# Performance work log

Measured on AMD Instinct MI355X. Metric: run time of the kernel, lower is better.

## Reference

```python
import jax, jax.numpy as jnp
import numpy as np

B, S, D, H = 4, 1024, 1024, 16
HD = D // H  # head_dim = 64


def setup_inputs() -> dict:
    key = jax.random.key(0)
    ks = jax.random.split(key, 12)
    inp = {
        "query": jax.random.normal(ks[0], (B, S, D), jnp.float32),
        "key": jax.random.normal(ks[1], (B, S, D), jnp.float32),
        "value": jax.random.normal(ks[2], (B, S, D), jnp.float32),
        # padding mask: 0 = masked, 1 = keep; broadcastable to [B,H,Sq,Sk]
        "mask": jax.random.randint(ks[3], (B, 1, 1, S), 0, 2, jnp.int32),
        # Dense params (Glorot-ish scale)
        "Wq": jax.random.normal(ks[4], (D, D), jnp.float32) / np.sqrt(D),
        "bq": jnp.zeros((D,), jnp.float32),
        "Wk": jax.random.normal(ks[5], (D, D), jnp.float32) / np.sqrt(D),
        "bk": jnp.zeros((D,), jnp.float32),
        "Wv": jax.random.normal(ks[6], (D, D), jnp.float32) / np.sqrt(D),
        "bv": jnp.zeros((D,), jnp.float32),
        "Wo": jax.random.normal(ks[7], (D, D), jnp.float32) / np.sqrt(D),
        "bo": jnp.zeros((D,), jnp.float32),
    }
    return inp


def _split_heads(x):
    # [B, S, D] -> [B, H, S, HD]
    b, s, _ = x.shape
    return x.reshape(b, s, H, HD).transpose(0, 2, 1, 3)


def reference(query, key, value, mask, Wq, bq, Wk, bk, Wv, bv, Wo, bo):
    q = _split_heads(query @ Wq + bq)   # [B,H,S,HD]
    k = _split_heads(key @ Wk + bk)
    v = _split_heads(value @ Wv + bv)

    scale = jnp.sqrt(jnp.asarray(HD, q.dtype))
    energy = jnp.einsum("bhqd,bhkd->bhqk", q, k) / scale  # [B,H,S,S]
    energy = jnp.where(mask == 0, jnp.asarray(-1e10, energy.dtype), energy)
    attention = jax.nn.softmax(energy, axis=-1)
    # dropout is identity at inference
    x = jnp.einsum("bhqk,bhkd->bhqd", attention, v)       # [B,H,S,HD]
    x = x.transpose(0, 2, 1, 3).reshape(query.shape[0], -1, H * HD)  # [B,S,D]
    outputs = x @ Wo + bo
    return outputs, attention
```

## Files before the change

kernel.cpp:

```cpp
#include <hip/hip_runtime.h>

typedef short short8  __attribute__((ext_vector_type(8)));
typedef short short4v __attribute__((ext_vector_type(4)));
typedef float float4v __attribute__((ext_vector_type(4)));
typedef int   int4v   __attribute__((ext_vector_type(4)));

__device__ __forceinline__ short f2bf(float f) {
    unsigned u = __builtin_bit_cast(unsigned, f);
    u += 0x7fff + ((u >> 16) & 1);
    return (short)(u >> 16);
}

__device__ __forceinline__ void gl_lds16(const void* g, void* l) {
    __builtin_amdgcn_global_load_lds(
        (const __attribute__((address_space(1))) void*)g,
        (__attribute__((address_space(3))) void*)l, 16, 0, 0);
}

__global__ __launch_bounds__(256) void prep(
    const float* __restrict__ W0, const float* __restrict__ W1,
    const float* __restrict__ W2, const float* __restrict__ W3,
    short* __restrict__ T0, short* __restrict__ T1,
    short* __restrict__ T2, short* __restrict__ T3,
    const float* __restrict__ qf, const float* __restrict__ kf,
    const float* __restrict__ vf,
    short* __restrict__ Qb, short* __restrict__ Kb, short* __restrict__ Vb)
{
    __shared__ short Tl[64 * 72];
    const int tid = threadIdx.x;
    if (blockIdx.x >= 1024) {
        int cid = blockIdx.x - 1024;
        int arr = cid >> 11;
        const float* src = arr == 0 ? qf : arr == 1 ? kf : vf;
        short*       dst = arr == 0 ? Qb : arr == 1 ? Kb : Vb;
        size_t base = ((size_t)(cid & 2047) * 256 + tid) * 8;
        float4v v0 = *(const float4v*)&src[base];
        float4v v1 = *(const float4v*)&src[base + 4];
        short8 o = {f2bf(v0[0]), f2bf(v0[1]), f2bf(v0[2]), f2bf(v0[3]),
                    f2bf(v1[0]), f2bf(v1[1]), f2bf(v1[2]), f2bf(v1[3])};
        *(short8*)&dst[base] = o;
        return;
    }
    const int mat = blockIdx.x >> 8;
    const int t   = blockIdx.x & 255;
    const int k0 = (t >> 4) * 64, n0 = (t & 15) * 64;
    const float* W = mat == 0 ? W0 : mat == 1 ? W1 : mat == 2 ? W2 : W3;
    short*       T = mat == 0 ? T0 : mat == 1 ? T1 : mat == 2 ? T2 : T3;
    #pragma unroll
    for (int i = 0; i < 4; i++) {
        int c = tid + i * 256;
        int row = c >> 4, c4 = (c & 15) * 4;
        float4v v = *(const float4v*)&W[(size_t)(k0 + row) * 1024 + n0 + c4];
        short4v s = {f2bf(v[0]), f2bf(v[1]), f2bf(v[2]), f2bf(v[3])};
        *(short4v*)&Tl[row * 72 + c4] = s;
    }
    __syncthreads();
    #pragma unroll
    for (int i = 0; i < 2; i++) {
        int c = tid + i * 256;
        int nrow = c >> 3, k8 = (c & 7) * 8;
        short8 v;
        #pragma unroll
        for (int e = 0; e < 8; e++) v[e] = Tl[(k8 + e) * 72 + nrow];
        *(short8*)&T[(size_t)(n0 + nrow) * 1024 + k0 + k8] = v;
    }
}

template<int CMODE>
__global__ __launch_bounds__(256) void gemm128(
    const short* __restrict__ A, const short* __restrict__ Bt,
    const float* __restrict__ bias, void* __restrict__ Cv,
    int M, int N, int K)
{
    __shared__ short As[128 * 64];
    __shared__ short Bs[64 * 64];
    const int tid = threadIdx.x;
    const int w = tid >> 6, lid = tid & 63, quad = lid >> 4, l15 = lid & 15;
    const int wr = w >> 1, wc = w & 1;
    const int m0 = blockIdx.x * 128, n0 = blockIdx.y * 64;
    const int lrow = lid >> 3;
    const int lcb  = lid & 7;

    float4v acc[4][2];
    #pragma unroll
    for (int i = 0; i < 4; i++)
        #pragma unroll
        for (int j = 0; j < 2; j++) acc[i][j] = (float4v){0.f, 0.f, 0.f, 0.f};

    for (int kb = 0; kb < K; kb += 64) {
        #pragma unroll
        for (int p = 0; p < 4; p++) {
            int chunk = p * 4 + w;
            int row = chunk * 8 + lrow;
            int cb = lcb ^ (row & 7);
            gl_lds16(&A[(size_t)(m0 + row) * K + kb + cb * 8], &As[chunk * 512]);
        }
        #pragma unroll
        for (int p = 0; p < 2; p++) {
            int chunk = p * 4 + w;
            int row = chunk * 8 + lrow;
            int cb = lcb ^ (row & 7);
            gl_lds16(&Bt[(size_t)(n0 + row) * K + kb + cb * 8], &Bs[chunk * 512]);
        }
        __syncthreads();

        short8 af[4][2], bfr[2][2];
        #pragma unroll
        for (int i = 0; i < 4; i++) {
            int row = wr * 64 + i * 16 + l15;
            int sw = row & 7;
            #pragma unroll
            for (int h = 0; h < 2; h++)
                af[i][h] = *(short8*)&As[row * 64 + ((h * 4 + quad) ^ sw) * 8];
        }
        #pragma unroll
        for (int j = 0; j < 2; j++) {
            int row = wc * 32 + j * 16 + l15;
            int sw = row & 7;
            #pragma unroll
            for (int h = 0; h < 2; h++)
                bfr[j][h] = *(short8*)&Bs[row * 64 + ((h * 4 + quad) ^ sw) * 8];
        }
        #pragma unroll
        for (int i = 0; i < 4; i++)
            #pragma unroll
            for (int j = 0; j < 2; j++) {
                acc[i][j] = __builtin_amdgcn_mfma_f32_16x16x32_bf16(
                    af[i][0], bfr[j][0], acc[i][j], 0, 0, 0);
                acc[i][j] = __builtin_amdgcn_mfma_f32_16x16x32_bf16(
                    af[i][1], bfr[j][1], acc[i][j], 0, 0, 0);
            }
        __syncthreads();
    }

    #pragma unroll
    for (int j = 0; j < 2; j++) {
        int n = n0 + wc * 32 + j * 16 + l15;
        float bj = bias[n];
        #pragma unroll
        for (int i = 0; i < 4; i++) {
            if constexpr (CMODE == 2) {
                short* Vt = (short*)Cv;
                int b = m0 >> 10;
                int sbase = (m0 & 1023) + wr * 64 + i * 16 + quad * 4;
                short4v sv;
                #pragma unroll
                for (int r = 0; r < 4; r++) sv[r] = f2bf(acc[i][j][r] + bj);
                *(short4v*)&Vt[(size_t)b * 1048576 + (size_t)n * 1024 + sbase] = sv;
            } else {
                #pragma unroll
                for (int r = 0; r < 4; r++) {
                    int m = m0 + wr * 64 + i * 16 + quad * 4 + r;
                    if constexpr (CMODE == 1)
                        ((float*)Cv)[(size_t)m * N + n] = acc[i][j][r] + bj;
                    else
                        ((short*)Cv)[(size_t)m * N + n] = f2bf(acc[i][j][r] + bj);
                }
            }
        }
    }
}

__global__ __launch_bounds__(256) void attn_kernel(
    const short* __restrict__ Qp, const short* __restrict__ Kp,
    const short* __restrict__ Vt, const int* __restrict__ mask,
    float* __restrict__ attnOut, short* __restrict__ X)
{
    __shared__ short KVl[128 * 72];
    __shared__ short Pl[16 * 136];
    __shared__ int   maskl[1024];
    __shared__ float redmx[4][16];
    __shared__ float redsm[4][16];

    const int tid = threadIdx.x;
    const int w = tid >> 6, lid = tid & 63, quad = lid >> 4, l15 = lid & 15;
    const int bid = blockIdx.x;
    const int qb = bid & 63;
    const int bh = bid >> 6;
    const int b = bh >> 4, h = bh & 15;
    const int q0 = qb * 16;
    const size_t rowbase = (size_t)b * 1048576;

    *(int4v*)&maskl[tid * 4] = *(const int4v*)&mask[b * 1024 + tid * 4];

    short8 aq0 = *(const short8*)
        &Qp[rowbase + (size_t)(q0 + l15) * 1024 + h * 64 + quad * 8];
    short8 aq1 = *(const short8*)
        &Qp[rowbase + (size_t)(q0 + l15) * 1024 + h * 64 + 32 + quad * 8];

    float4v accS[16];
    #pragma unroll
    for (int a = 0; a < 16; a++) accS[a] = (float4v){0.f, 0.f, 0.f, 0.f};

    for (int nk = 0; nk < 8; nk++) {
        #pragma unroll
        for (int i = 0; i < 4; i++) {
            int c = tid + i * 256;
            int row = c >> 3, k8 = (c & 7) * 8;
            *(short8*)&KVl[row * 72 + k8] = *(const short8*)
                &Kp[rowbase + (size_t)(nk * 128 + row) * 1024 + h * 64 + k8];
        }
        __syncthreads();
        #pragma unroll
        for (int jj = 0; jj < 2; jj++) {
            int nloc = w * 32 + jj * 16 + l15;
            short8 b0 = *(short8*)&KVl[nloc * 72 + quad * 8];
            short8 b1 = *(short8*)&KVl[nloc * 72 + 32 + quad * 8];
            int a = nk * 2 + jj;
            accS[a] = __builtin_amdgcn_mfma_f32_16x16x32_bf16(aq0, b0, accS[a], 0, 0, 0);
            accS[a] = __builtin_amdgcn_mfma_f32_16x16x32_bf16(aq1, b1, accS[a], 0, 0, 0);
        }
        __syncthreads();
    }

    float mx[4] = {-3e38f, -3e38f, -3e38f, -3e38f};
    #pragma unroll
    for (int a = 0; a < 16; a++) {
        int col = (a >> 1) * 128 + w * 32 + (a & 1) * 16 + l15;
        bool keep = maskl[col] != 0;
        #pragma unroll
        for (int r = 0; r < 4; r++) {
            float s = accS[a][r] * 0.125f;
            s = keep ? s : -1e10f;
            accS[a][r] = s;
            mx[r] = fmaxf(mx[r], s);
        }
    }
    #pragma unroll
    for (int off = 1; off < 16; off <<= 1)
        #pragma unroll
        for (int r = 0; r < 4; r++) mx[r] = fmaxf(mx[r], __shfl_xor(mx[r], off));
    if (l15 == 0) {
        #pragma unroll
        for (int r = 0; r < 4; r++) redmx[w][quad * 4 + r] = mx[r];
    }
    __syncthreads();
    float mrow[4], sm[4] = {0.f, 0.f, 0.f, 0.f};
    #pragma unroll
    for (int r = 0; r < 4; r++) {
        int qr = quad * 4 + r;
        mrow[r] = fmaxf(fmaxf(redmx[0][qr], redmx[1][qr]),
                        fmaxf(redmx[2][qr], redmx[3][qr]));
    }
    #pragma unroll
    for (int a = 0; a < 16; a++)
        #pragma unroll
        for (int r = 0; r < 4; r++) {
            float e = __expf(accS[a][r] - mrow[r]);
            accS[a][r] = e;
            sm[r] += e;
        }
    #pragma unroll
    for (int off = 1; off < 16; off <<= 1)
        #pragma unroll
        for (int r = 0; r < 4; r++) sm[r] += __shfl_xor(sm[r], off);
    if (l15 == 0) {
        #pragma unroll
        for (int r = 0; r < 4; r++) redsm[w][quad * 4 + r] = sm[r];
    }
    __syncthreads();
    float inv[4];
    #pragma unroll
    for (int r = 0; r < 4; r++) {
        int qr = quad * 4 + r;
        inv[r] = 1.0f / (redsm[0][qr] + redsm[1][qr] + redsm[2][qr] + redsm[3][qr]);
    }

    const size_t abase = ((size_t)bh * 1024 + q0) * 1024;
    float4v accX = (float4v){0.f, 0.f, 0.f, 0.f};
    for (int kt = 0; kt < 8; kt++) {
        #pragma unroll
        for (int i = 0; i < 4; i++) {
            int c = tid + i * 256;
            int row = c >> 4, s8 = (c & 15) * 8;
            *(short8*)&KVl[row * 136 + s8] = *(const short8*)
                &Vt[rowbase + (size_t)(h * 64 + row) * 1024 + kt * 128 + s8];
        }
        #pragma unroll
        for (int jj = 0; jj < 2; jj++) {
            int a = kt * 2 + jj;
            int cl = w * 32 + jj * 16 + l15;
            int col = kt * 128 + cl;
            #pragma unroll
            for (int r = 0; r < 4; r++) {
                float p = accS[a][r] * inv[r];
                attnOut[abase + (size_t)(quad * 4 + r) * 1024 + col] = p;
                Pl[(quad * 4 + r) * 136 + cl] = f2bf(p);
            }
        }
        __syncthreads();
        #pragma unroll
        for (int kk = 0; kk < 4; kk++) {
            short8 ap = *(short8*)&Pl[l15 * 136 + kk * 32 + quad * 8];
            short8 bv = *(short8*)&KVl[(w * 16 + l15) * 136 + kk * 32 + quad * 8];
            accX = __builtin_amdgcn_mfma_f32_16x16x32_bf16(ap, bv, accX, 0, 0, 0);
        }
        __syncthreads();
    }
    #pragma unroll
    for (int r = 0; r < 4; r++)
        X[rowbase + (size_t)(q0 + quad * 4 + r) * 1024 + h * 64 + w * 16 + l15] =
            f2bf(accX[r]);
}

extern "C" void kernel_launch(void* const* d_in, const int* in_sizes, int n_in,
                              void* d_out, int out_size, void* d_ws, size_t ws_size,
                              hipStream_t stream)
{
    const float* q_in = (const float*)d_in[0];
    const float* k_in = (const float*)d_in[1];
    const float* v_in = (const float*)d_in[2];
    const int*   mask = (const int*)d_in[3];
    const float* Wq = (const float*)d_in[4];
    const float* bq = (const float*)d_in[5];
    const float* Wk = (const float*)d_in[6];
    const float* bk = (const float*)d_in[7];
    const float* Wv = (const float*)d_in[8];
    const float* bv = (const float*)d_in[9];
    const float* Wo = (const float*)d_in[10];
    const float* bo = (const float*)d_in[11];

    short* ws = (short*)d_ws;
    const size_t MEL = 4096ull * 1024;
    short* Qp  = ws;
    short* Kp  = ws + MEL;
    short* Vt  = ws + 2 * MEL;
    short* Xp  = ws + 3 * MEL;
    short* WqT = ws + 4 * MEL;
    short* WkT = WqT + 1024 * 1024;
    short* WvT = WkT + 1024 * 1024;
    short* WoT = WvT + 1024 * 1024;

    float* outp  = (float*)d_out;
    float* attnp = outp + MEL;

    short* Qb = (short*)attnp;
    short* Kb = Qb + MEL;
    short* Vb = Kb + MEL;

    prep<<<dim3(7168), dim3(256), 0, stream>>>(Wq, Wk, Wv, Wo,
                                               WqT, WkT, WvT, WoT,
                                               q_in, k_in, v_in, Qb, Kb, Vb);
    dim3 gg(32, 16);
    gemm128<0><<<gg, 256, 0, stream>>>(Qb, WqT, bq, Qp, 4096, 1024, 1024);
    gemm128<0><<<gg, 256, 0, stream>>>(Kb, WkT, bk, Kp, 4096, 1024, 1024);
    gemm128<2><<<gg, 256, 0, stream>>>(Vb, WvT, bv, Vt, 4096, 1024, 1024);
    attn_kernel<<<dim3(4096), dim3(256), 0, stream>>>(Qp, Kp, Vt, mask, attnp, Xp);
    gemm128<1><<<gg, 256, 0, stream>>>(Xp, WoT, bo, outp, 4096, 1024, 1024);
}
```

Before: 542.2 us.

## Load K/V operands directly from global and split PV across waves with LDS reduction

```diff
diff --git a/kernel.cpp b/kernel.cpp
--- a/kernel.cpp
+++ b/kernel.cpp
@@ -166,11 +166,11 @@
     const short* __restrict__ Vt, const int* __restrict__ mask,
     float* __restrict__ attnOut, short* __restrict__ X)
 {
-    __shared__ short KVl[128 * 72];
-    __shared__ short Pl[16 * 136];
+    __shared__ short Pl[4][16][32];
     __shared__ int   maskl[1024];
     __shared__ float redmx[4][16];
     __shared__ float redsm[4][16];
+    __shared__ float Xr[4][16][64];
 
     const int tid = threadIdx.x;
     const int w = tid >> 6, lid = tid & 63, quad = lid >> 4, l15 = lid & 15;
@@ -180,38 +180,33 @@
     const int b = bh >> 4, h = bh & 15;
     const int q0 = qb * 16;
     const size_t rowbase = (size_t)b * 1048576;
+    const size_t hoff = (size_t)h * 64;
 
     *(int4v*)&maskl[tid * 4] = *(const int4v*)&mask[b * 1024 + tid * 4];
 
     short8 aq0 = *(const short8*)
-        &Qp[rowbase + (size_t)(q0 + l15) * 1024 + h * 64 + quad * 8];
+        &Qp[rowbase + (size_t)(q0 + l15) * 1024 + hoff + quad * 8];
     short8 aq1 = *(const short8*)
-        &Qp[rowbase + (size_t)(q0 + l15) * 1024 + h * 64 + 32 + quad * 8];
+        &Qp[rowbase + (size_t)(q0 + l15) * 1024 + hoff + 32 + quad * 8];
 
     float4v accS[16];
     #pragma unroll
     for (int a = 0; a < 16; a++) accS[a] = (float4v){0.f, 0.f, 0.f, 0.f};
 
+    #pragma unroll
     for (int nk = 0; nk < 8; nk++) {
         #pragma unroll
-        for (int i = 0; i < 4; i++) {
-            int c = tid + i * 256;
-            int row = c >> 3, k8 = (c & 7) * 8;
-            *(short8*)&KVl[row * 72 + k8] = *(const short8*)
-                &Kp[rowbase + (size_t)(nk * 128 + row) * 1024 + h * 64 + k8];
-        }
-        __syncthreads();
-        #pragma unroll
         for (int jj = 0; jj < 2; jj++) {
-            int nloc = w * 32 + jj * 16 + l15;
-            short8 b0 = *(short8*)&KVl[nloc * 72 + quad * 8];
-            short8 b1 = *(short8*)&KVl[nloc * 72 + 32 + quad * 8];
+            int n = nk * 128 + w * 32 + jj * 16 + l15;
+            const short* kr = &Kp[rowbase + (size_t)n * 1024 + hoff + quad * 8];
+            short8 b0 = *(const short8*)kr;
+            short8 b1 = *(const short8*)(kr + 32);
             int a = nk * 2 + jj;
             accS[a] = __builtin_amdgcn_mfma_f32_16x16x32_bf16(aq0, b0, accS[a], 0, 0, 0);
             accS[a] = __builtin_amdgcn_mfma_f32_16x16x32_bf16(aq1, b1, accS[a], 0, 0, 0);
         }
-        __syncthreads();
-    }
+    }
+    __syncthreads();
 
     float mx[4] = {-3e38f, -3e38f, -3e38f, -3e38f};
     #pragma unroll
@@ -267,40 +262,50 @@
     }
 
     const size_t abase = ((size_t)bh * 1024 + q0) * 1024;
-    float4v accX = (float4v){0.f, 0.f, 0.f, 0.f};
+    float4v accXp[4];
+    #pragma unroll
+    for (int jj = 0; jj < 4; jj++) accXp[jj] = (float4v){0.f, 0.f, 0.f, 0.f};
+
     for (int kt = 0; kt < 8; kt++) {
         #pragma unroll
-        for (int i = 0; i < 4; i++) {
-            int c = tid + i * 256;
-            int row = c >> 4, s8 = (c & 15) * 8;
-            *(short8*)&KVl[row * 136 + s8] = *(const short8*)
-                &Vt[rowbase + (size_t)(h * 64 + row) * 1024 + kt * 128 + s8];
-        }
-        #pragma unroll
-        for (int jj = 0; jj < 2; jj++) {
-            int a = kt * 2 + jj;
-            int cl = w * 32 + jj * 16 + l15;
-            int col = kt * 128 + cl;
+        for (int jj2 = 0; jj2 < 2; jj2++) {
+            int a = kt * 2 + jj2;
+            int col = kt * 128 + w * 32 + jj2 * 16 + l15;
             #pragma unroll
             for (int r = 0; r < 4; r++) {
                 float p = accS[a][r] * inv[r];
                 attnOut[abase + (size_t)(quad * 4 + r) * 1024 + col] = p;
-                Pl[(quad * 4 + r) * 136 + cl] = f2bf(p);
+                Pl[w][quad * 4 + r][jj2 * 16 + l15] = f2bf(p);
             }
         }
-        __syncthreads();
-        #pragma unroll
-        for (int kk = 0; kk < 4; kk++) {
-            short8 ap = *(short8*)&Pl[l15 * 136 + kk * 32 + quad * 8];
-            short8 bv = *(short8*)&KVl[(w * 16 + l15) * 136 + kk * 32 + quad * 8];
-            accX = __builtin_amdgcn_mfma_f32_16x16x32_bf16(ap, bv, accX, 0, 0, 0);
-        }
-        __syncthreads();
-    }
-    #pragma unroll
-    for (int r = 0; r < 4; r++)
-        X[rowbase + (size_t)(q0 + quad * 4 + r) * 1024 + h * 64 + w * 16 + l15] =
-            f2bf(accX[r]);
+        short8 ap = *(short8*)&Pl[w][l15][quad * 8];
+        #pragma unroll
+        for (int jj = 0; jj < 4; jj++) {
+            short8 bv = *(const short8*)
+                &Vt[rowbase + (hoff + jj * 16 + l15) * 1024 +
+                    kt * 128 + w * 32 + quad * 8];
+            accXp[jj] = __builtin_amdgcn_mfma_f32_16x16x32_bf16(ap, bv, accXp[jj], 0, 0, 0);
+        }
+    }
+
+    #pragma unroll
+    for (int jj = 0; jj < 4; jj++)
+        #pragma unroll
+        for (int r = 0; r < 4; r++)
+            Xr[w][quad * 4 + r][jj * 16 + l15] = accXp[jj][r];
+    __syncthreads();
+    {
+        int q = tid >> 4, d4 = (tid & 15) * 4;
+        float4v s0 = *(float4v*)&Xr[0][q][d4];
+        float4v s1 = *(float4v*)&Xr[1][q][d4];
+        float4v s2 = *(float4v*)&Xr[2][q][d4];
+        float4v s3 = *(float4v*)&Xr[3][q][d4];
+        short4v o;
+        #pragma unroll
+        for (int e = 0; e < 4; e++)
+            o[e] = f2bf(s0[e] + s1[e] + s2[e] + s3[e]);
+        *(short4v*)&X[rowbase + (size_t)(q0 + q) * 1024 + hoff + d4] = o;
+    }
 }
 
 extern "C" void kernel_launch(void* const* d_in, const int* in_sizes, int n_in,
```

Result: faster. 529.6 us (-2.3%).
